# Kernel tuning notes

Measured on AMD Instinct MI355X. Metric: run time of the kernel, lower is better.

## Reference

```python
import jax, jax.numpy as jnp
import numpy as np

# SpikingLayer config (init_kwargs)
THRESHOLD = 1.0
THRESHOLD_LOW = -1.0
MEMBRANE_SUBTRACT = 1.0  # membrane_subtract=None -> defaults to threshold
WINDOW = 1.0             # module-level `window = 1.0`; surrogate window = threshold * window
BATCH = 16

# sinabs ThresholdSubtract: forward emits floor(v/threshold) spikes when v > 0,
# backward uses a boxcar surrogate gradient over [threshold - window, inf).
@jax.custom_vjp
def threshold_subtract(state):
    return jnp.where(state > 0, jnp.floor(state / THRESHOLD), 0.0).astype(state.dtype)

def _ts_fwd(state):
    return threshold_subtract(state), state

def _ts_bwd(state, g):
    surrogate = (state >= (THRESHOLD - WINDOW)).astype(g.dtype)
    return (g * surrogate / THRESHOLD,)

threshold_subtract.defvjp(_ts_fwd, _ts_bwd)


def setup_inputs() -> dict:
    key = jax.random.key(0)
    # (batch*time, C, H, W) = (16*128, 32, 32, 32); scale to [0,2) so spikes occur
    x = jax.random.uniform(key, (2048, 32, 32, 32), dtype=jnp.float32) * 2.0
    return {"binary_input": x}


def reference(binary_input):
    feat = binary_input.shape[1:]
    # (B*T, *feat) -> (B, T, *feat) -> (T, B, *feat)
    syn = jnp.swapaxes(binary_input.reshape(BATCH, -1, *feat), 0, 1)
    state0 = jnp.zeros(syn.shape[1:], syn.dtype)
    act0 = jnp.zeros(syn.shape[1:], syn.dtype)

    def step(carry, syn_t):
        state, act = carry
        # membrane_reset=False: subtract spikes * membrane_subtract
        state = syn_t + state - act * MEMBRANE_SUBTRACT
        # lower bound clamp: relu(v - th_low) + th_low
        state = jnp.maximum(state - THRESHOLD_LOW, 0.0) + THRESHOLD_LOW
        act = threshold_subtract(state)
        return (state, act), act

    _, spikes = jax.lax.scan(step, (state0, act0), syn)  # (T, B, *feat)
    T = spikes.shape[0]
    # (T, B, *feat) -> (B, T, *feat) -> (B*T, *feat)
    return jnp.swapaxes(spikes, 0, 1).reshape(BATCH * T, *feat)
```

## Files before the change

kernel.cpp:

```cpp
#include <hip/hip_runtime.h>


constexpr int T_STEPS = 128;
constexpr int FEAT    = 32 * 32 * 32;
constexpr int FEATQ   = FEAT / 4;

__global__ __launch_bounds__(256) void spiking_scan_kernel(
    const float4* __restrict__ in, float4* __restrict__ out)
{
    const int idx = blockIdx.x * 256 + threadIdx.x;
    const int b   = idx >> 13;
    const int f   = idx & (FEATQ - 1);
    const size_t base = (size_t)b * T_STEPS * FEATQ + (size_t)f;
    const float4* __restrict__ src = in  + base;
    float4*       __restrict__ dst = out + base;

    float s0 = 0.f, s1 = 0.f, s2 = 0.f, s3 = 0.f;
    float a0 = 0.f, a1 = 0.f, a2 = 0.f, a3 = 0.f;

    #pragma unroll 4
    for (int t = 0; t < T_STEPS; ++t) {
        const float4 syn = src[(size_t)t * FEATQ];

        s0 = (syn.x + s0) - a0;
        s1 = (syn.y + s1) - a1;
        s2 = (syn.z + s2) - a2;
        s3 = (syn.w + s3) - a3;

        s0 = fmaxf(s0 + 1.0f, 0.0f) - 1.0f;
        s1 = fmaxf(s1 + 1.0f, 0.0f) - 1.0f;
        s2 = fmaxf(s2 + 1.0f, 0.0f) - 1.0f;
        s3 = fmaxf(s3 + 1.0f, 0.0f) - 1.0f;

        a0 = (s0 > 0.0f) ? floorf(s0) : 0.0f;
        a1 = (s1 > 0.0f) ? floorf(s1) : 0.0f;
        a2 = (s2 > 0.0f) ? floorf(s2) : 0.0f;
        a3 = (s3 > 0.0f) ? floorf(s3) : 0.0f;

        float4 o;
        o.x = a0; o.y = a1; o.z = a2; o.w = a3;
        dst[(size_t)t * FEATQ] = o;
    }
}

extern "C" void kernel_launch(void* const* d_in, const int* in_sizes, int n_in,
                              void* d_out, int out_size, void* d_ws, size_t ws_size,
                              hipStream_t stream)
{
    (void)in_sizes; (void)n_in; (void)d_ws; (void)ws_size; (void)out_size;
    const float4* in  = (const float4*)d_in[0];
    float4*       out = (float4*)d_out;

    const int total_quads = 16 * FEATQ;
    const int block = 256;
    const int grid  = total_quads / block;
    spiking_scan_kernel<<<grid, block, 0, stream>>>(in, out);
}
```

Before: 438.8 us.

## Use scalar per-thread scan with double-buffered chunked prefetch and nontemporal access

Each thread now handles one scalar feature instead of a float4, which gives four times as many threads to hide memory latency. Input loads are issued in chunks of 8 timesteps and double-buffered, so the next chunk is in flight while the current one is computed. Loads and stores use nontemporal builtins to avoid cache pollution on this streaming pass. In exchange, accesses become 4-byte per lane instead of 16-byte vectors, and register use per thread goes up.

```diff
diff --git a/kernel.cpp b/kernel.cpp
--- a/kernel.cpp
+++ b/kernel.cpp
@@ -3,43 +3,54 @@
 
 constexpr int T_STEPS = 128;
 constexpr int FEAT    = 32 * 32 * 32;
-constexpr int FEATQ   = FEAT / 4;
+constexpr int CHUNK   = 8;
+constexpr int NCHUNK  = T_STEPS / CHUNK;
 
 __global__ __launch_bounds__(256) void spiking_scan_kernel(
-    const float4* __restrict__ in, float4* __restrict__ out)
+    const float* __restrict__ in, float* __restrict__ out)
 {
     const int idx = blockIdx.x * 256 + threadIdx.x;
-    const int b   = idx >> 13;
-    const int f   = idx & (FEATQ - 1);
-    const size_t base = (size_t)b * T_STEPS * FEATQ + (size_t)f;
-    const float4* __restrict__ src = in  + base;
-    float4*       __restrict__ dst = out + base;
+    const int b   = idx >> 15;
+    const int f   = idx & (FEAT - 1);
+    const size_t base = (size_t)b * T_STEPS * FEAT + (size_t)f;
+    const float* __restrict__ src = in  + base;
+    float*       __restrict__ dst = out + base;
 
-    float s0 = 0.f, s1 = 0.f, s2 = 0.f, s3 = 0.f;
-    float a0 = 0.f, a1 = 0.f, a2 = 0.f, a3 = 0.f;
+    float s = 0.f, a = 0.f;
+    float bufA[CHUNK], bufB[CHUNK];
 
-    #pragma unroll 4
-    for (int t = 0; t < T_STEPS; ++t) {
-        const float4 syn = src[(size_t)t * FEATQ];
+    #pragma unroll
+    for (int u = 0; u < CHUNK; ++u)
+        bufA[u] = __builtin_nontemporal_load(&src[(size_t)u * FEAT]);
 
-        s0 = (syn.x + s0) - a0;
-        s1 = (syn.y + s1) - a1;
-        s2 = (syn.z + s2) - a2;
-        s3 = (syn.w + s3) - a3;
+    for (int c = 0; c < NCHUNK; c += 2) {
+        #pragma unroll
+        for (int u = 0; u < CHUNK; ++u)
+            bufB[u] = __builtin_nontemporal_load(
+                &src[(size_t)((c + 1) * CHUNK + u) * FEAT]);
 
-        s0 = fmaxf(s0 + 1.0f, 0.0f) - 1.0f;
-        s1 = fmaxf(s1 + 1.0f, 0.0f) - 1.0f;
-        s2 = fmaxf(s2 + 1.0f, 0.0f) - 1.0f;
-        s3 = fmaxf(s3 + 1.0f, 0.0f) - 1.0f;
+        #pragma unroll
+        for (int u = 0; u < CHUNK; ++u) {
+            s = (bufA[u] + s) - a;
+            s = fmaxf(s + 1.0f, 0.0f) - 1.0f;
+            a = (s > 0.0f) ? floorf(s) : 0.0f;
+            __builtin_nontemporal_store(a, &dst[(size_t)(c * CHUNK + u) * FEAT]);
+        }
 
-        a0 = (s0 > 0.0f) ? floorf(s0) : 0.0f;
-        a1 = (s1 > 0.0f) ? floorf(s1) : 0.0f;
-        a2 = (s2 > 0.0f) ? floorf(s2) : 0.0f;
-        a3 = (s3 > 0.0f) ? floorf(s3) : 0.0f;
+        if (c + 2 < NCHUNK) {
+            #pragma unroll
+            for (int u = 0; u < CHUNK; ++u)
+                bufA[u] = __builtin_nontemporal_load(
+                    &src[(size_t)((c + 2) * CHUNK + u) * FEAT]);
+        }
 
-        float4 o;
-        o.x = a0; o.y = a1; o.z = a2; o.w = a3;
-        dst[(size_t)t * FEATQ] = o;
+        #pragma unroll
+        for (int u = 0; u < CHUNK; ++u) {
+            s = (bufB[u] + s) - a;
+            s = fmaxf(s + 1.0f, 0.0f) - 1.0f;
+            a = (s > 0.0f) ? floorf(s) : 0.0f;
+            __builtin_nontemporal_store(a, &dst[(size_t)((c + 1) * CHUNK + u) * FEAT]);
+        }
     }
 }
 
@@ -48,11 +59,11 @@
                               hipStream_t stream)
 {
     (void)in_sizes; (void)n_in; (void)d_ws; (void)ws_size; (void)out_size;
-    const float4* in  = (const float4*)d_in[0];
-    float4*       out = (float4*)d_out;
+    const float* in  = (const float*)d_in[0];
+    float*       out = (float*)d_out;
 
-    const int total_quads = 16 * FEATQ;
+    const int total = 16 * FEAT;
     const int block = 256;
-    const int grid  = total_quads / block;
+    const int grid  = total / block;
     spiking_scan_kernel<<<grid, block, 0, stream>>>(in, out);
 }
```

Result: faster. 422.1 us (-3.8%).
